# Performance work log

Measured on AMD Instinct MI355X. Metric: run time of the kernel, lower is better.

## Reference

```python
import jax, jax.numpy as jnp
import numpy as np
import math

B, S = 4, 1024
N_ITEMS, EMB = 50000, 128
H, D = 4, 32


def setup_inputs() -> dict:
    key = jax.random.key(0)
    ks = jax.random.split(key, 12)

    def lin(k, fan_in, fan_out):
        lim = 1.0 / math.sqrt(fan_in)
        return jax.random.uniform(k, (fan_in, fan_out), minval=-lim, maxval=lim, dtype=jnp.float32)

    inp = {}
    inp["sequence_item_indices"] = jax.random.randint(ks[0], (B, S), 0, N_ITEMS, dtype=jnp.int32)
    inp["sequence_correct_flags"] = jax.random.randint(ks[1], (B, S), 0, 2, dtype=jnp.int32)
    inp["sequence_time_gaps"] = jax.random.uniform(ks[2], (B, S), dtype=jnp.float32) * 100.0
    inp["item_emb"] = jax.random.normal(ks[3], (N_ITEMS, EMB), dtype=jnp.float32) * 0.02
    inp["ans_emb"] = jax.random.normal(ks[4], (2, EMB), dtype=jnp.float32) * 0.02
    inp["Wq"] = lin(ks[5], EMB, H * D); inp["bq"] = jnp.zeros((H * D,), jnp.float32)
    inp["Wk"] = lin(ks[6], EMB, H * D); inp["bk"] = jnp.zeros((H * D,), jnp.float32)
    inp["Wv"] = lin(ks[7], EMB, H * D); inp["bv"] = jnp.zeros((H * D,), jnp.float32)
    inp["Wh"] = lin(ks[8], 2 * EMB, EMB); inp["bh"] = jnp.zeros((EMB,), jnp.float32)
    inp["W1"] = lin(ks[9], H * D + EMB, EMB); inp["b1"] = jnp.zeros((EMB,), jnp.float32)
    inp["W2"] = lin(ks[10], EMB, 1); inp["b2"] = jnp.zeros((1,), jnp.float32)
    inp["theta_raw"] = jnp.zeros((H,), jnp.float32)
    return inp


def reference(sequence_item_indices, sequence_correct_flags, sequence_time_gaps,
              item_emb, ans_emb, Wq, bq, Wk, bk, Wv, bv, Wh, bh, W1, b1, W2, b2, theta_raw):
    Bb, Ss = sequence_item_indices.shape
    Hn = theta_raw.shape[0]
    Dd = Wq.shape[1] // Hn

    e = item_emb[sequence_item_indices]                      # [B,S,E]
    a = ans_emb[sequence_correct_flags]                      # [B,S,E]
    inter = jnp.concatenate([e, a], axis=-1) @ Wh + bh       # history_projection

    Q = (e @ Wq + bq).reshape(Bb, Ss, Hn, Dd)
    K = (e @ Wk + bk).reshape(Bb, Ss, Hn, Dd)
    V = (inter @ Wv + bv).reshape(Bb, Ss, Hn, Dd)
    scale = 1.0 / jnp.sqrt(jnp.float32(Dd))

    # self relevance per history position; per-target softmax over i<t done via exclusive prefix sums
    sr = jnp.sum(Q * K, axis=-1) * scale                     # [B,S,H]
    ex = jnp.exp(sr - jnp.max(sr, axis=1, keepdims=True))    # shift-invariant
    Ep = jnp.concatenate([jnp.zeros((Bb, 1, Hn), sr.dtype), jnp.cumsum(ex, axis=1)], axis=1)  # [B,S+1,H]

    g = jnp.maximum(sequence_time_gaps.astype(jnp.float32), 1.0)
    Pp = jnp.concatenate([jnp.zeros((Bb, 1), g.dtype), jnp.cumsum(g, axis=1)], axis=1)        # [B,S+1]

    t = jnp.arange(1, Ss)                                    # targets, T = S-1
    i = jnp.arange(Ss)                                       # history positions
    mask = i[None, :] < t[:, None]                           # [T,S]
    step = (t[:, None] - i[None, :]).astype(jnp.float32)     # arange(L,0,-1)[i] == t - i
    gap_diff = Pp[:, 1:Ss, None] - Pp[:, None, :Ss]          # [B,T,S]  sum_{j in [i,t)} clamp(gap,1)
    Et = Ep[:, 1:Ss, :]                                      # [B,T,H]  softmax normalizer Z_t
    rel = (Et[:, :, None, :] - Ep[:, None, :Ss, :]) / Et[:, :, None, :]  # cumulative relevance [B,T,S,H]
    pd = jnp.where(mask[None, :, :, None],
                   step[None, :, :, None] * gap_diff[..., None] * rel, 0.0)  # perceived distance

    theta = jax.nn.softplus(theta_raw) + 1e-4                # [H]
    decay = jnp.exp(-theta * pd)                             # [B,T,S,H]

    # candidate query at position t equals query_projection(item_embedding[t])
    raw = jnp.einsum('bthd,bihd->btih', Q[:, 1:], K) * scale # [B,T,S,H]
    scores = jnp.where(mask[None, :, :, None], raw * decay, -1e30)
    attn = jax.nn.softmax(scores, axis=2)                    # softmax over history positions
    ctx = jnp.einsum('btih,bihd->bthd', attn, V).reshape(Bb, Ss - 1, Hn * Dd)

    feat = jnp.concatenate([ctx, e[:, 1:]], axis=-1)
    h1 = jax.nn.relu(feat @ W1 + b1)                         # dropout is inference identity
    logit = (h1 @ W2 + b2)[..., 0]
    pred = jax.nn.sigmoid(logit)                             # [B,S-1]
    valid = jnp.ones((Bb, Ss - 1), dtype=bool)               # all positions valid (no padding)
    return pred, valid
```

## Files before the change

### kernel.cpp

```cpp
#include <hip/hip_runtime.h>
#include <math.h>

#define BSZ 4
#define SSZ 1024
#define EMBD 128
#define HN 4
#define DN 32
#define TQ (SSZ - 1)
#define NROWS (BSZ * TQ)

typedef __attribute__((ext_vector_type(8))) short bf16x8;
typedef __attribute__((ext_vector_type(4))) short bf16x4;
typedef __attribute__((ext_vector_type(4))) float f32x4;

static __device__ __forceinline__ unsigned short f2bf(float x) {
    union { float f; unsigned u; } v; v.f = x;
    unsigned r = v.u + 0x7fffu + ((v.u >> 16) & 1u);
    return (unsigned short)(r >> 16);
}
static __device__ __forceinline__ bf16x8 cvt8(const float4 a, const float4 b) {
    bf16x8 v;
    v[0] = (short)f2bf(a.x); v[1] = (short)f2bf(a.y);
    v[2] = (short)f2bf(a.z); v[3] = (short)f2bf(a.w);
    v[4] = (short)f2bf(b.x); v[5] = (short)f2bf(b.y);
    v[6] = (short)f2bf(b.z); v[7] = (short)f2bf(b.w);
    return v;
}

__global__ __launch_bounds__(256)
void embed4_kernel(const int* __restrict__ idx, const int* __restrict__ flg,
                   const float* __restrict__ item_emb, const float* __restrict__ ans_emb,
                   const float* __restrict__ Wq, const float* __restrict__ bq,
                   const float* __restrict__ Wk, const float* __restrict__ bk,
                   const float* __restrict__ Wv, const float* __restrict__ bv,
                   const float* __restrict__ Wh, const float* __restrict__ bh_bias,
                   unsigned short* __restrict__ Qts, unsigned short* __restrict__ Kts,
                   unsigned short* __restrict__ Vts,
                   float* __restrict__ ec, float* __restrict__ srw)
{
    __shared__ __align__(16) unsigned short esb[16][136];
    __shared__ __align__(16) unsigned short asb[16][136];
    __shared__ __align__(16) unsigned short intb[16][136];
    __shared__ __align__(16) unsigned short Wt[128][40];

    const int tid = threadIdx.x;
    const int tok0 = blockIdx.x * 16;
    const int b = blockIdx.x >> 6;
    const int s0 = tok0 & 1023;
    const int w = tid >> 6, lane = tid & 63;
    const int quad = lane >> 4, col = lane & 15;

    {
        const int tk = tid >> 4;
        const int d0 = (tid & 15) * 8;
        const int tok = tok0 + tk;
        const float* esrc = item_emb + (size_t)idx[tok] * EMBD + d0;
        const float* asrc = ans_emb + (size_t)flg[tok] * EMBD + d0;
        const float4 e0 = *(const float4*)esrc;
        const float4 e1 = *(const float4*)(esrc + 4);
        const float4 a0 = *(const float4*)asrc;
        const float4 a1 = *(const float4*)(asrc + 4);
        *(float4*)(ec + (size_t)tok * EMBD + d0) = e0;
        *(float4*)(ec + (size_t)tok * EMBD + d0 + 4) = e1;
        *(bf16x8*)&esb[tk][d0] = cvt8(e0, e1);
        *(bf16x8*)&asb[tk][d0] = cvt8(a0, a1);
    }

    const int jb = (tid & 31) * 4;
    const int ib = (tid >> 5) * 4;
    float rr[4][4];

    #define WSRC(R) ((R) < 8 ? Wh + (size_t)(R) * 4096                     \
                  : (R) < 12 ? Wq + (size_t)((R) - 8) * 4096               \
                  : (R) < 16 ? Wk + (size_t)((R) - 12) * 4096              \
                  : Wv + (size_t)((R) - 16) * 4096)
    #define LOADW(P)                                                       \
    {                                                                      \
        const float* _p = (P);                                             \
        *(float4*)rr[0] = *(const float4*)(_p + (ib + 0) * 128 + jb);      \
        *(float4*)rr[1] = *(const float4*)(_p + (ib + 1) * 128 + jb);      \
        *(float4*)rr[2] = *(const float4*)(_p + (ib + 2) * 128 + jb);      \
        *(float4*)rr[3] = *(const float4*)(_p + (ib + 3) * 128 + jb);      \
    }
    #define STOREW                                                         \
    {                                                                      \
        _Pragma("unroll")                                                  \
        for (int jj = 0; jj < 4; jj++) {                                   \
            bf16x4 v;                                                      \
            v[0] = (short)f2bf(rr[0][jj]); v[1] = (short)f2bf(rr[1][jj]);  \
            v[2] = (short)f2bf(rr[2][jj]); v[3] = (short)f2bf(rr[3][jj]);  \
            *(bf16x4*)&Wt[jb + jj][ib] = v;                                \
        }                                                                  \
    }

    f32x4 accI[2] = {{0.f,0.f,0.f,0.f},{0.f,0.f,0.f,0.f}};
    f32x4 accQ[2] = {{0.f,0.f,0.f,0.f},{0.f,0.f,0.f,0.f}};
    f32x4 accK[2] = {{0.f,0.f,0.f,0.f},{0.f,0.f,0.f,0.f}};
    f32x4 accV[2] = {{0.f,0.f,0.f,0.f},{0.f,0.f,0.f,0.f}};

    LOADW(WSRC(0));
    #pragma unroll
    for (int r = 0; r < 20; r++) {
        __syncthreads();
        STOREW;
        __syncthreads();
        if (r < 19) LOADW(WSRC(r + 1));

        const unsigned short (*Ab)[136] = (r < 4) ? esb : (r < 8) ? asb
                                        : (r < 16) ? esb : intb;
        const int koff = ((r < 8) ? (r & 3) : (r < 12) ? (r - 8)
                        : (r < 16) ? (r - 12) : (r - 16)) * 32;
        const bf16x8 af = *(const bf16x8*)&Ab[col][koff + quad * 8];
        f32x4* acc = (r < 8) ? accI : (r < 12) ? accQ : (r < 16) ? accK : accV;
        #pragma unroll
        for (int ntl = 0; ntl < 2; ntl++) {
            const bf16x8 bf = *(const bf16x8*)&Wt[w * 32 + ntl * 16 + col][quad * 8];
            acc[ntl] = __builtin_amdgcn_mfma_f32_16x16x32_bf16(af, bf, acc[ntl], 0, 0, 0);
        }
        if (r == 7) {
            #pragma unroll
            for (int ntl = 0; ntl < 2; ntl++) {
                const int j = w * 32 + ntl * 16 + col;
                const float bb = bh_bias[j];
                #pragma unroll
                for (int r4 = 0; r4 < 4; r4++)
                    intb[quad * 4 + r4][j] = f2bf(accI[ntl][r4] + bb);
            }
        }
    }
    #undef LOADW
    #undef STOREW
    #undef WSRC

    const int bhn = b * HN + w;
    const float scale = 0.17677669529663687f;
    float p[4] = {0.f, 0.f, 0.f, 0.f};
    #pragma unroll
    for (int ntl = 0; ntl < 2; ntl++) {
        const int j = w * 32 + ntl * 16 + col;
        const float bQ = bq[j], bK = bk[j], bV = bv[j];
        #pragma unroll
        for (int r = 0; r < 4; r++) {
            const float qv = accQ[ntl][r] + bQ;
            const float kv = accK[ntl][r] + bK;
            const int s = s0 + quad * 4 + r;
            const size_t o = ((size_t)bhn * SSZ + s) * DN + ntl * 16 + col;
            Qts[o] = f2bf(qv * scale);
            Kts[o] = f2bf(kv);
            Vts[o] = f2bf(accV[ntl][r] + bV);
            p[r] = fmaf(qv, kv, p[r]);
        }
    }
    #pragma unroll
    for (int r = 0; r < 4; r++) {
        float pr = p[r];
        pr += __shfl_xor(pr, 1, 64);
        pr += __shfl_xor(pr, 2, 64);
        pr += __shfl_xor(pr, 4, 64);
        pr += __shfl_xor(pr, 8, 64);
        if (col == 0)
            srw[(size_t)bhn * SSZ + s0 + quad * 4 + r] = pr * scale;
    }
}

__global__ __launch_bounds__(256)
void attn4_kernel(const unsigned short* __restrict__ Qts,
                  const unsigned short* __restrict__ Kts,
                  const unsigned short* __restrict__ Vts,
                  const float* __restrict__ srw, const float* __restrict__ gaps,
                  const float* __restrict__ theta_raw, float* __restrict__ csw)
{
    __shared__ __align__(16) unsigned short Ks[64][40];
    __shared__ __align__(16) unsigned short Vs[32][72];
    __shared__ __align__(16) unsigned short Ps[4][16][72];
    __shared__ float EpS[SSZ + 1];
    __shared__ float PpS[SSZ + 1];
    __shared__ float wtot[4];

    const int bid = blockIdx.x;
    const int qt = bid & 15;
    const int bh = bid >> 4;
    const int b = bh >> 2, h = bh & 3;
    const int tid = threadIdx.x;
    const int w = tid >> 6, lane = tid & 63;
    const int quad = lane >> 4, col = lane & 15;
    const int t0 = qt * 64 + 1;

    {
        const float4 sv = *(const float4*)(srw + (size_t)bh * SSZ + tid * 4);
        const float e0 = __expf(sv.x);
        const float p0 = e0;
        const float p1 = p0 + __expf(sv.y);
        const float p2 = p1 + __expf(sv.z);
        const float p3 = p2 + __expf(sv.w);
        float s = p3;
        #pragma unroll
        for (int d = 1; d < 64; d <<= 1) {
            const float t = __shfl_up(s, d, 64);
            if (lane >= d) s += t;
        }
        if (lane == 63) wtot[w] = s;
        __syncthreads();
        float base = s - p3;
        for (int ww = 0; ww < w; ww++) base += wtot[ww];
        EpS[tid * 4 + 1] = base + p0;
        EpS[tid * 4 + 2] = base + p1;
        EpS[tid * 4 + 3] = base + p2;
        EpS[tid * 4 + 4] = base + p3;
        if (tid == 0) EpS[0] = 0.0f;
    }
    {
        const float4 gv = *(const float4*)(gaps + (size_t)b * SSZ + tid * 4);
        const float p0 = fmaxf(gv.x, 1.0f);
        const float p1 = p0 + fmaxf(gv.y, 1.0f);
        const float p2 = p1 + fmaxf(gv.z, 1.0f);
        const float p3 = p2 + fmaxf(gv.w, 1.0f);
        float s = p3;
        #pragma unroll
        for (int d = 1; d < 64; d <<= 1) {
            const float t = __shfl_up(s, d, 64);
            if (lane >= d) s += t;
        }
        __syncthreads();
        if (lane == 63) wtot[w] = s;
        __syncthreads();
        float base = s - p3;
        for (int ww = 0; ww < w; ww++) base += wtot[ww];
        PpS[tid * 4 + 1] = base + p0;
        PpS[tid * 4 + 2] = base + p1;
        PpS[tid * 4 + 3] = base + p2;
        PpS[tid * 4 + 4] = base + p3;
        if (tid == 0) PpS[0] = 0.0f;
    }
    __syncthreads();

    const float theta = logf(1.0f + __expf(theta_raw[h])) + 1e-4f;
    const float nth = -theta;
    float Ept[4], Ppt[4], iEp[4], tft[4];
    int qrow[4], tq[4];
    #pragma unroll
    for (int r = 0; r < 4; r++) {
        qrow[r] = w * 16 + quad * 4 + r;
        tq[r] = t0 + qrow[r];
        tft[r] = (float)tq[r];
        Ept[r] = EpS[tq[r]];
        Ppt[r] = PpS[tq[r]];
        iEp[r] = 1.0f / Ept[r];
    }

    bf16x8 aq;
    {
        int t = t0 + w * 16 + col; if (t > 1023) t = 1023;
        aq = *(const bf16x8*)(Qts + ((size_t)(bh * SSZ + t)) * DN + quad * 8);
    }

    f32x4 acc0 = {0.f, 0.f, 0.f, 0.f};
    f32x4 acc1 = {0.f, 0.f, 0.f, 0.f};
    float lsum[4] = {0.f, 0.f, 0.f, 0.f};

    const int i_st = tid >> 2;
    const int d0 = (tid & 3) * 8;
    bf16x8 kreg = *(const bf16x8*)(Kts + ((size_t)(bh * SSZ + i_st)) * DN + d0);
    bf16x8 vreg = *(const bf16x8*)(Vts + ((size_t)(bh * SSZ + i_st)) * DN + d0);

    for (int c = 0; c <= qt; c++) {
        __syncthreads();
        *(bf16x8*)&Ks[i_st][d0] = kreg;
        #pragma unroll
        for (int k2 = 0; k2 < 8; k2++) Vs[d0 + k2][i_st] = (unsigned short)vreg[k2];
        __syncthreads();
        if (c < qt) {
            const size_t o = ((size_t)(bh * SSZ + (c + 1) * 64 + i_st)) * DN + d0;
            kreg = *(const bf16x8*)(Kts + o);
            vreg = *(const bf16x8*)(Vts + o);
        }

        const bool full = (c < qt);
        #pragma unroll
        for (int nt = 0; nt < 4; nt++) {
            const bf16x8 bk = *(const bf16x8*)&Ks[nt * 16 + col][quad * 8];
            f32x4 z = {0.f, 0.f, 0.f, 0.f};
            f32x4 raw = __builtin_amdgcn_mfma_f32_16x16x32_bf16(aq, bk, z, 0, 0, 0);
            const int il = nt * 16 + col;
            const int i_ = c * 64 + il;
            const float Epi = EpS[i_];
            const float Ppi = PpS[i_];
            const float fi = (float)i_;
            #pragma unroll
            for (int r = 0; r < 4; r++) {
                const float pdv = (tft[r] - fi) * (Ppt[r] - Ppi) * ((Ept[r] - Epi) * iEp[r]);
                const float sc  = raw[r] * __expf(nth * pdv);
                float p = __expf(sc);
                p = (full || il <= qrow[r]) ? p : 0.0f;
                lsum[r] += p;
                Ps[w][quad * 4 + r][il] = f2bf(p);
            }
        }
        #pragma unroll
        for (int ks = 0; ks < 2; ks++) {
            const bf16x8 ap = *(const bf16x8*)&Ps[w][col][ks * 32 + quad * 8];
            const bf16x8 bv0 = *(const bf16x8*)&Vs[col][ks * 32 + quad * 8];
            const bf16x8 bv1 = *(const bf16x8*)&Vs[16 + col][ks * 32 + quad * 8];
            acc0 = __builtin_amdgcn_mfma_f32_16x16x32_bf16(ap, bv0, acc0, 0, 0, 0);
            acc1 = __builtin_amdgcn_mfma_f32_16x16x32_bf16(ap, bv1, acc1, 0, 0, 0);
        }
    }

    #pragma unroll
    for (int r = 0; r < 4; r++) {
        float lr = lsum[r];
        #pragma unroll
        for (int msk = 8; msk >= 1; msk >>= 1) lr += __shfl_xor(lr, msk, 64);
        lsum[r] = 1.0f / lr;
    }
    #pragma unroll
    for (int r = 0; r < 4; r++) {
        if (tq[r] <= 1023) {
            float* dst = csw + ((size_t)(b * TQ + (tq[r] - 1))) * EMBD + h * DN;
            dst[col]      = acc0[r] * lsum[r];
            dst[16 + col] = acc1[r] * lsum[r];
        }
    }
}

__global__ __launch_bounds__(256)
void mlp3_kernel(const float* __restrict__ csw, const float* __restrict__ ec,
                 const float* __restrict__ W1, const float* __restrict__ b1,
                 const float* __restrict__ W2, const float* __restrict__ b2,
                 float* __restrict__ out)
{
    __shared__ __align__(16) unsigned short featb[32][264];
    __shared__ __align__(16) unsigned short W1t[128][264];
    __shared__ float sred[4][16];

    const int tid = threadIdx.x;
    const int r0 = blockIdx.x * 32;
    const int w = tid >> 6, lane = tid & 63;
    const int quad = lane >> 4, col = lane & 15;
    const int mt = w & 1, nh = w >> 1;

    {
        const int jb = (tid & 31) * 4;
        const int ib = (tid >> 5) * 4;
        for (int ic = 0; ic < 8; ic++) {
            const int i0 = ic * 32 + ib;
            float rr[4][4];
            *(float4*)rr[0] = *(const float4*)(W1 + (size_t)(i0 + 0) * 128 + jb);
            *(float4*)rr[1] = *(const float4*)(W1 + (size_t)(i0 + 1) * 128 + jb);
            *(float4*)rr[2] = *(const float4*)(W1 + (size_t)(i0 + 2) * 128 + jb);
            *(float4*)rr[3] = *(const float4*)(W1 + (size_t)(i0 + 3) * 128 + jb);
            #pragma unroll
            for (int jj = 0; jj < 4; jj++) {
                bf16x4 v;
                v[0] = (short)f2bf(rr[0][jj]); v[1] = (short)f2bf(rr[1][jj]);
                v[2] = (short)f2bf(rr[2][jj]); v[3] = (short)f2bf(rr[3][jj]);
                *(bf16x4*)&W1t[jb + jj][i0] = v;
            }
        }
    }
    {
        const int rr = tid >> 3;
        const int c0 = (tid & 7) * 32;
        int row = r0 + rr; if (row >= NROWS) row = NROWS - 1;
        const float* src;
        if (c0 < 128) {
            src = csw + (size_t)row * EMBD + c0;
        } else {
            const int bb = row / TQ;
            const int tt = row - bb * TQ + 1;
            src = ec + ((size_t)(bb * SSZ + tt)) * EMBD + (c0 - 128);
        }
        #pragma unroll
        for (int g = 0; g < 4; g++) {
            const float4 f0 = ((const float4*)src)[g * 2];
            const float4 f1 = ((const float4*)src)[g * 2 + 1];
            *(bf16x8*)&featb[rr][c0 + g * 8] = cvt8(f0, f1);
        }
    }
    __syncthreads();

    float s[4] = {0.f, 0.f, 0.f, 0.f};
    #pragma unroll
    for (int ntl = 0; ntl < 4; ntl++) {
        const int nt = nh * 4 + ntl;
        f32x4 acc = {0.f, 0.f, 0.f, 0.f};
        #pragma unroll
        for (int kc = 0; kc < 8; kc++) {
            const bf16x8 af = *(const bf16x8*)&featb[mt * 16 + col][kc * 32 + quad * 8];
            const bf16x8 bf = *(const bf16x8*)&W1t[nt * 16 + col][kc * 32 + quad * 8];
            acc = __builtin_amdgcn_mfma_f32_16x16x32_bf16(af, bf, acc, 0, 0, 0);
        }
        const int j = nt * 16 + col;
        const float b1j = b1[j], w2j = W2[j];
        #pragma unroll
        for (int r = 0; r < 4; r++)
            s[r] = fmaf(fmaxf(acc[r] + b1j, 0.0f), w2j, s[r]);
    }
    #pragma unroll
    for (int r = 0; r < 4; r++) {
        float sr = s[r];
        sr += __shfl_xor(sr, 1, 64);
        sr += __shfl_xor(sr, 2, 64);
        sr += __shfl_xor(sr, 4, 64);
        sr += __shfl_xor(sr, 8, 64);
        if (col == 0) sred[w][quad * 4 + r] = sr;
    }
    __syncthreads();
    if (tid < 32) {
        const int mt2 = tid >> 4, rr = tid & 15;
        const float logit = sred[mt2][rr] + sred[mt2 + 2][rr] + b2[0];
        const int grow = r0 + tid;
        if (grow < NROWS) {
            out[grow] = 1.0f / (1.0f + __expf(-logit));
            out[NROWS + grow] = 1.0f;
        }
    }
}

extern "C" void kernel_launch(void* const* d_in, const int* in_sizes, int n_in,
                              void* d_out, int out_size, void* d_ws, size_t ws_size,
                              hipStream_t stream)
{
    const int*   idx       = (const int*)d_in[0];
    const int*   flg       = (const int*)d_in[1];
    const float* gaps      = (const float*)d_in[2];
    const float* item_emb  = (const float*)d_in[3];
    const float* ans_emb   = (const float*)d_in[4];
    const float* Wq        = (const float*)d_in[5];
    const float* bq        = (const float*)d_in[6];
    const float* Wk        = (const float*)d_in[7];
    const float* bk        = (const float*)d_in[8];
    const float* Wv        = (const float*)d_in[9];
    const float* bv        = (const float*)d_in[10];
    const float* Wh        = (const float*)d_in[11];
    const float* bh        = (const float*)d_in[12];
    const float* W1        = (const float*)d_in[13];
    const float* b1        = (const float*)d_in[14];
    const float* W2        = (const float*)d_in[15];
    const float* b2        = (const float*)d_in[16];
    const float* theta_raw = (const float*)d_in[17];
    (void)in_sizes; (void)n_in; (void)ws_size;

    const size_t QKV = (size_t)BSZ * HN * SSZ * DN;
    unsigned short* Qts = (unsigned short*)d_ws;
    unsigned short* Kts = Qts + QKV;
    unsigned short* Vts = Kts + QKV;
    float* ec  = (float*)(Vts + QKV);
    float* srw = ec + (size_t)BSZ * SSZ * EMBD;
    float* csw = srw + (size_t)BSZ * HN * SSZ;

    float* out = (float*)d_out;

    embed4_kernel<<<BSZ * SSZ / 16, 256, 0, stream>>>(
        idx, flg, item_emb, ans_emb, Wq, bq, Wk, bk, Wv, bv, Wh, bh,
        Qts, Kts, Vts, ec, srw);
    attn4_kernel<<<BSZ * HN * 16, 256, 0, stream>>>(
        Qts, Kts, Vts, srw, gaps, theta_raw, csw);
    mlp3_kernel<<<(NROWS + 31) / 32, 256, 0, stream>>>(
        csw, ec, W1, b1, W2, b2, out);
}
```

Before: 149.4 us.

## Split attention key chunks across waves, double-buffer embed weights, shrink MLP tiles

The attention kernel no longer has all four waves share each 64-key chunk. Each wave now processes its own interleaved key chunks for all 64 queries of the block, with private K/V/P tiles, and the partial outputs and normalizers are merged through shared-memory atomics. This removes the per-chunk block-wide barriers and the serial chunk loop. The embed kernel double-buffers the transposed weight tile so there is one barrier per step instead of two, and the MLP kernel moves to 16-row tiles where each wave stages only its own slice of W1. The costs are more shared memory, LDS atomics, and W1 being converted twice as many times overall.

```diff
diff --git a/kernel.cpp b/kernel.cpp
--- a/kernel.cpp
+++ b/kernel.cpp
@@ -28,7 +28,7 @@
 }
 
 __global__ __launch_bounds__(256)
-void embed4_kernel(const int* __restrict__ idx, const int* __restrict__ flg,
+void embed5_kernel(const int* __restrict__ idx, const int* __restrict__ flg,
                    const float* __restrict__ item_emb, const float* __restrict__ ans_emb,
                    const float* __restrict__ Wq, const float* __restrict__ bq,
                    const float* __restrict__ Wk, const float* __restrict__ bk,
@@ -41,7 +41,7 @@
     __shared__ __align__(16) unsigned short esb[16][136];
     __shared__ __align__(16) unsigned short asb[16][136];
     __shared__ __align__(16) unsigned short intb[16][136];
-    __shared__ __align__(16) unsigned short Wt[128][40];
+    __shared__ __align__(16) unsigned short Wt[2][128][40];
 
     const int tid = threadIdx.x;
     const int tok0 = blockIdx.x * 16;
@@ -82,14 +82,14 @@
         *(float4*)rr[2] = *(const float4*)(_p + (ib + 2) * 128 + jb);      \
         *(float4*)rr[3] = *(const float4*)(_p + (ib + 3) * 128 + jb);      \
     }
-    #define STOREW                                                         \
+    #define STOREW(B)                                                      \
     {                                                                      \
         _Pragma("unroll")                                                  \
         for (int jj = 0; jj < 4; jj++) {                                   \
             bf16x4 v;                                                      \
             v[0] = (short)f2bf(rr[0][jj]); v[1] = (short)f2bf(rr[1][jj]);  \
             v[2] = (short)f2bf(rr[2][jj]); v[3] = (short)f2bf(rr[3][jj]);  \
-            *(bf16x4*)&Wt[jb + jj][ib] = v;                                \
+            *(bf16x4*)&Wt[B][jb + jj][ib] = v;                             \
         }                                                                  \
     }
 
@@ -99,11 +99,11 @@
     f32x4 accV[2] = {{0.f,0.f,0.f,0.f},{0.f,0.f,0.f,0.f}};
 
     LOADW(WSRC(0));
+    STOREW(0);
+    __syncthreads();
+
     #pragma unroll
     for (int r = 0; r < 20; r++) {
-        __syncthreads();
-        STOREW;
-        __syncthreads();
         if (r < 19) LOADW(WSRC(r + 1));
 
         const unsigned short (*Ab)[136] = (r < 4) ? esb : (r < 8) ? asb
@@ -114,7 +114,7 @@
         f32x4* acc = (r < 8) ? accI : (r < 12) ? accQ : (r < 16) ? accK : accV;
         #pragma unroll
         for (int ntl = 0; ntl < 2; ntl++) {
-            const bf16x8 bf = *(const bf16x8*)&Wt[w * 32 + ntl * 16 + col][quad * 8];
+            const bf16x8 bf = *(const bf16x8*)&Wt[r & 1][w * 32 + ntl * 16 + col][quad * 8];
             acc[ntl] = __builtin_amdgcn_mfma_f32_16x16x32_bf16(af, bf, acc[ntl], 0, 0, 0);
         }
         if (r == 7) {
@@ -127,6 +127,8 @@
                     intb[quad * 4 + r4][j] = f2bf(accI[ntl][r4] + bb);
             }
         }
+        if (r < 19) STOREW((r + 1) & 1);
+        __syncthreads();
     }
     #undef LOADW
     #undef STOREW
@@ -164,18 +166,19 @@
 }
 
 __global__ __launch_bounds__(256)
-void attn4_kernel(const unsigned short* __restrict__ Qts,
+void attn5_kernel(const unsigned short* __restrict__ Qts,
                   const unsigned short* __restrict__ Kts,
                   const unsigned short* __restrict__ Vts,
                   const float* __restrict__ srw, const float* __restrict__ gaps,
                   const float* __restrict__ theta_raw, float* __restrict__ csw)
 {
-    __shared__ __align__(16) unsigned short Ks[64][40];
-    __shared__ __align__(16) unsigned short Vs[32][72];
-    __shared__ __align__(16) unsigned short Ps[4][16][72];
+    __shared__ __align__(16) unsigned short Kw[4][64][40];
+    __shared__ __align__(16) unsigned short Vw[4][32][72];
+    __shared__ __align__(16) unsigned short Pw[4][64][72];
     __shared__ float EpS[SSZ + 1];
-    __shared__ float PpS[SSZ + 1];
+    __shared__ float PpS[SSZ + 2];
     __shared__ float wtot[4];
+    __shared__ float mrg[64][36];
 
     const int bid = blockIdx.x;
     const int qt = bid & 15;
@@ -186,10 +189,11 @@
     const int quad = lane >> 4, col = lane & 15;
     const int t0 = qt * 64 + 1;
 
+    for (int x = tid; x < 64 * 36; x += 256) ((float*)mrg)[x] = 0.0f;
+
     {
         const float4 sv = *(const float4*)(srw + (size_t)bh * SSZ + tid * 4);
-        const float e0 = __expf(sv.x);
-        const float p0 = e0;
+        const float p0 = __expf(sv.x);
         const float p1 = p0 + __expf(sv.y);
         const float p2 = p1 + __expf(sv.z);
         const float p3 = p2 + __expf(sv.w);
@@ -237,130 +241,144 @@
     const float theta = logf(1.0f + __expf(theta_raw[h])) + 1e-4f;
     const float nth = -theta;
     float Ept[4], Ppt[4], iEp[4], tft[4];
-    int qrow[4], tq[4];
-    #pragma unroll
-    for (int r = 0; r < 4; r++) {
-        qrow[r] = w * 16 + quad * 4 + r;
-        tq[r] = t0 + qrow[r];
-        tft[r] = (float)tq[r];
-        Ept[r] = EpS[tq[r]];
-        Ppt[r] = PpS[tq[r]];
-        iEp[r] = 1.0f / Ept[r];
-    }
-
-    bf16x8 aq;
-    {
-        int t = t0 + w * 16 + col; if (t > 1023) t = 1023;
-        aq = *(const bf16x8*)(Qts + ((size_t)(bh * SSZ + t)) * DN + quad * 8);
-    }
-
-    f32x4 acc0 = {0.f, 0.f, 0.f, 0.f};
-    f32x4 acc1 = {0.f, 0.f, 0.f, 0.f};
+    int qrow[4];
+    #pragma unroll
+    for (int nt = 0; nt < 4; nt++) {
+        qrow[nt] = nt * 16 + col;
+        const int t = t0 + qrow[nt];
+        tft[nt] = (float)t;
+        const int tc = (t <= 1023) ? t : 1023;
+        Ept[nt] = EpS[tc];
+        Ppt[nt] = PpS[tc];
+        iEp[nt] = 1.0f / Ept[nt];
+    }
+
+    bf16x8 bq[4];
+    #pragma unroll
+    for (int nt = 0; nt < 4; nt++) {
+        int t = t0 + nt * 16 + col; if (t > 1023) t = 1023;
+        bq[nt] = *(const bf16x8*)(Qts + ((size_t)(bh * SSZ + t)) * DN + quad * 8);
+    }
+
+    f32x4 acc[4][2];
+    #pragma unroll
+    for (int m = 0; m < 4; m++) { acc[m][0] = {0,0,0,0}; acc[m][1] = {0,0,0,0}; }
     float lsum[4] = {0.f, 0.f, 0.f, 0.f};
 
-    const int i_st = tid >> 2;
-    const int d0 = (tid & 3) * 8;
-    bf16x8 kreg = *(const bf16x8*)(Kts + ((size_t)(bh * SSZ + i_st)) * DN + d0);
-    bf16x8 vreg = *(const bf16x8*)(Vts + ((size_t)(bh * SSZ + i_st)) * DN + d0);
-
-    for (int c = 0; c <= qt; c++) {
-        __syncthreads();
-        *(bf16x8*)&Ks[i_st][d0] = kreg;
-        #pragma unroll
-        for (int k2 = 0; k2 < 8; k2++) Vs[d0 + k2][i_st] = (unsigned short)vreg[k2];
-        __syncthreads();
-        if (c < qt) {
-            const size_t o = ((size_t)(bh * SSZ + (c + 1) * 64 + i_st)) * DN + d0;
-            kreg = *(const bf16x8*)(Kts + o);
-            vreg = *(const bf16x8*)(Vts + o);
+    bf16x8 kpre[4], vpre[4];
+    {
+        const size_t o = ((size_t)(bh * SSZ + w * 64 + lane)) * DN;
+        #pragma unroll
+        for (int j = 0; j < 4; j++) {
+            kpre[j] = *(const bf16x8*)(Kts + o + j * 8);
+            vpre[j] = *(const bf16x8*)(Vts + o + j * 8);
+        }
+    }
+
+    for (int c = w; c <= qt; c += 4) {
+        #pragma unroll
+        for (int j = 0; j < 4; j++) *(bf16x8*)&Kw[w][lane][j * 8] = kpre[j];
+        #pragma unroll
+        for (int j = 0; j < 4; j++)
+            #pragma unroll
+            for (int k = 0; k < 8; k++) Vw[w][j * 8 + k][lane] = (unsigned short)vpre[j][k];
+        if (c + 4 <= qt) {
+            const size_t o = ((size_t)(bh * SSZ + (c + 4) * 64 + lane)) * DN;
+            #pragma unroll
+            for (int j = 0; j < 4; j++) {
+                kpre[j] = *(const bf16x8*)(Kts + o + j * 8);
+                vpre[j] = *(const bf16x8*)(Vts + o + j * 8);
+            }
         }
 
         const bool full = (c < qt);
         #pragma unroll
-        for (int nt = 0; nt < 4; nt++) {
-            const bf16x8 bk = *(const bf16x8*)&Ks[nt * 16 + col][quad * 8];
-            f32x4 z = {0.f, 0.f, 0.f, 0.f};
-            f32x4 raw = __builtin_amdgcn_mfma_f32_16x16x32_bf16(aq, bk, z, 0, 0, 0);
-            const int il = nt * 16 + col;
-            const int i_ = c * 64 + il;
-            const float Epi = EpS[i_];
-            const float Ppi = PpS[i_];
-            const float fi = (float)i_;
+        for (int mt = 0; mt < 4; mt++) {
+            const bf16x8 af = *(const bf16x8*)&Kw[w][mt * 16 + col][quad * 8];
+            f32x4 raw[4];
+            #pragma unroll
+            for (int nt = 0; nt < 4; nt++) {
+                f32x4 z = {0.f, 0.f, 0.f, 0.f};
+                raw[nt] = __builtin_amdgcn_mfma_f32_16x16x32_bf16(af, bq[nt], z, 0, 0, 0);
+            }
             #pragma unroll
             for (int r = 0; r < 4; r++) {
-                const float pdv = (tft[r] - fi) * (Ppt[r] - Ppi) * ((Ept[r] - Epi) * iEp[r]);
-                const float sc  = raw[r] * __expf(nth * pdv);
-                float p = __expf(sc);
-                p = (full || il <= qrow[r]) ? p : 0.0f;
-                lsum[r] += p;
-                Ps[w][quad * 4 + r][il] = f2bf(p);
-            }
-        }
-        #pragma unroll
-        for (int ks = 0; ks < 2; ks++) {
-            const bf16x8 ap = *(const bf16x8*)&Ps[w][col][ks * 32 + quad * 8];
-            const bf16x8 bv0 = *(const bf16x8*)&Vs[col][ks * 32 + quad * 8];
-            const bf16x8 bv1 = *(const bf16x8*)&Vs[16 + col][ks * 32 + quad * 8];
-            acc0 = __builtin_amdgcn_mfma_f32_16x16x32_bf16(ap, bv0, acc0, 0, 0, 0);
-            acc1 = __builtin_amdgcn_mfma_f32_16x16x32_bf16(ap, bv1, acc1, 0, 0, 0);
-        }
-    }
-
-    #pragma unroll
-    for (int r = 0; r < 4; r++) {
-        float lr = lsum[r];
-        #pragma unroll
-        for (int msk = 8; msk >= 1; msk >>= 1) lr += __shfl_xor(lr, msk, 64);
-        lsum[r] = 1.0f / lr;
-    }
-    #pragma unroll
-    for (int r = 0; r < 4; r++) {
-        if (tq[r] <= 1023) {
-            float* dst = csw + ((size_t)(b * TQ + (tq[r] - 1))) * EMBD + h * DN;
-            dst[col]      = acc0[r] * lsum[r];
-            dst[16 + col] = acc1[r] * lsum[r];
+                const int kl = mt * 16 + quad * 4 + r;
+                const int i_ = c * 64 + kl;
+                const float Epi = EpS[i_];
+                const float Ppi = PpS[i_];
+                const float fi = (float)i_;
+                #pragma unroll
+                for (int nt = 0; nt < 4; nt++) {
+                    const float pdv = (tft[nt] - fi) * (Ppt[nt] - Ppi)
+                                    * ((Ept[nt] - Epi) * iEp[nt]);
+                    const float sc = raw[nt][r] * __expf(nth * pdv);
+                    float p = __expf(sc);
+                    p = (full || kl <= qrow[nt]) ? p : 0.0f;
+                    lsum[nt] += p;
+                    Pw[w][nt * 16 + col][kl] = f2bf(p);
+                }
+            }
+        }
+        #pragma unroll
+        for (int mtq = 0; mtq < 4; mtq++) {
+            #pragma unroll
+            for (int kc = 0; kc < 2; kc++) {
+                const bf16x8 ap = *(const bf16x8*)&Pw[w][mtq * 16 + col][kc * 32 + quad * 8];
+                const bf16x8 bv0 = *(const bf16x8*)&Vw[w][col][kc * 32 + quad * 8];
+                const bf16x8 bv1 = *(const bf16x8*)&Vw[w][16 + col][kc * 32 + quad * 8];
+                acc[mtq][0] = __builtin_amdgcn_mfma_f32_16x16x32_bf16(ap, bv0, acc[mtq][0], 0, 0, 0);
+                acc[mtq][1] = __builtin_amdgcn_mfma_f32_16x16x32_bf16(ap, bv1, acc[mtq][1], 0, 0, 0);
+            }
+        }
+    }
+
+    #pragma unroll
+    for (int nt = 0; nt < 4; nt++) {
+        float l = lsum[nt];
+        l += __shfl_xor(l, 16, 64);
+        l += __shfl_xor(l, 32, 64);
+        if (quad == 0) atomicAdd(&mrg[nt * 16 + col][32], l);
+    }
+    #pragma unroll
+    for (int mtq = 0; mtq < 4; mtq++)
+        #pragma unroll
+        for (int ntv = 0; ntv < 2; ntv++)
+            #pragma unroll
+            for (int r = 0; r < 4; r++)
+                atomicAdd(&mrg[mtq * 16 + quad * 4 + r][ntv * 16 + col], acc[mtq][ntv][r]);
+    __syncthreads();
+
+    {
+        const int q = tid >> 2, dg = tid & 3;
+        const int t = t0 + q;
+        if (t <= 1023) {
+            const float inv = 1.0f / mrg[q][32];
+            float* dst = csw + ((size_t)(b * TQ + (t - 1))) * EMBD + h * DN + dg * 8;
+            #pragma unroll
+            for (int d = 0; d < 8; d++) dst[d] = mrg[q][dg * 8 + d] * inv;
         }
     }
 }
 
 __global__ __launch_bounds__(256)
-void mlp3_kernel(const float* __restrict__ csw, const float* __restrict__ ec,
+void mlp4_kernel(const float* __restrict__ csw, const float* __restrict__ ec,
                  const float* __restrict__ W1, const float* __restrict__ b1,
                  const float* __restrict__ W2, const float* __restrict__ b2,
                  float* __restrict__ out)
 {
-    __shared__ __align__(16) unsigned short featb[32][264];
-    __shared__ __align__(16) unsigned short W1t[128][264];
+    __shared__ __align__(16) unsigned short featb[16][264];
+    __shared__ __align__(16) unsigned short W1q[4][32][264];
     __shared__ float sred[4][16];
 
     const int tid = threadIdx.x;
-    const int r0 = blockIdx.x * 32;
+    const int r0 = blockIdx.x * 16;
     const int w = tid >> 6, lane = tid & 63;
     const int quad = lane >> 4, col = lane & 15;
-    const int mt = w & 1, nh = w >> 1;
-
-    {
-        const int jb = (tid & 31) * 4;
-        const int ib = (tid >> 5) * 4;
-        for (int ic = 0; ic < 8; ic++) {
-            const int i0 = ic * 32 + ib;
-            float rr[4][4];
-            *(float4*)rr[0] = *(const float4*)(W1 + (size_t)(i0 + 0) * 128 + jb);
-            *(float4*)rr[1] = *(const float4*)(W1 + (size_t)(i0 + 1) * 128 + jb);
-            *(float4*)rr[2] = *(const float4*)(W1 + (size_t)(i0 + 2) * 128 + jb);
-            *(float4*)rr[3] = *(const float4*)(W1 + (size_t)(i0 + 3) * 128 + jb);
-            #pragma unroll
-            for (int jj = 0; jj < 4; jj++) {
-                bf16x4 v;
-                v[0] = (short)f2bf(rr[0][jj]); v[1] = (short)f2bf(rr[1][jj]);
-                v[2] = (short)f2bf(rr[2][jj]); v[3] = (short)f2bf(rr[3][jj]);
-                *(bf16x4*)&W1t[jb + jj][i0] = v;
-            }
-        }
-    }
-    {
-        const int rr = tid >> 3;
-        const int c0 = (tid & 7) * 32;
+
+    {
+        const int rr = tid >> 4;
+        const int c0 = (tid & 15) * 16;
         int row = r0 + rr; if (row >= NROWS) row = NROWS - 1;
         const float* src;
         if (c0 < 128) {
@@ -370,27 +388,47 @@
             const int tt = row - bb * TQ + 1;
             src = ec + ((size_t)(bb * SSZ + tt)) * EMBD + (c0 - 128);
         }
-        #pragma unroll
-        for (int g = 0; g < 4; g++) {
-            const float4 f0 = ((const float4*)src)[g * 2];
-            const float4 f1 = ((const float4*)src)[g * 2 + 1];
-            *(bf16x8*)&featb[rr][c0 + g * 8] = cvt8(f0, f1);
+        const float4 f0 = ((const float4*)src)[0];
+        const float4 f1 = ((const float4*)src)[1];
+        const float4 f2 = ((const float4*)src)[2];
+        const float4 f3 = ((const float4*)src)[3];
+        *(bf16x8*)&featb[rr][c0]     = cvt8(f0, f1);
+        *(bf16x8*)&featb[rr][c0 + 8] = cvt8(f2, f3);
+    }
+
+    {
+        const int jl = (lane & 7) * 4;
+        const int ib2 = (lane >> 3) * 4;
+        const int jg = w * 32 + jl;
+        for (int ic = 0; ic < 8; ic++) {
+            const int i0 = ic * 32 + ib2;
+            float rr[4][4];
+            *(float4*)rr[0] = *(const float4*)(W1 + (size_t)(i0 + 0) * 128 + jg);
+            *(float4*)rr[1] = *(const float4*)(W1 + (size_t)(i0 + 1) * 128 + jg);
+            *(float4*)rr[2] = *(const float4*)(W1 + (size_t)(i0 + 2) * 128 + jg);
+            *(float4*)rr[3] = *(const float4*)(W1 + (size_t)(i0 + 3) * 128 + jg);
+            #pragma unroll
+            for (int jj = 0; jj < 4; jj++) {
+                bf16x4 v;
+                v[0] = (short)f2bf(rr[0][jj]); v[1] = (short)f2bf(rr[1][jj]);
+                v[2] = (short)f2bf(rr[2][jj]); v[3] = (short)f2bf(rr[3][jj]);
+                *(bf16x4*)&W1q[w][jl + jj][i0] = v;
+            }
         }
     }
     __syncthreads();
 
     float s[4] = {0.f, 0.f, 0.f, 0.f};
     #pragma unroll
-    for (int ntl = 0; ntl < 4; ntl++) {
-        const int nt = nh * 4 + ntl;
+    for (int ntl = 0; ntl < 2; ntl++) {
         f32x4 acc = {0.f, 0.f, 0.f, 0.f};
         #pragma unroll
         for (int kc = 0; kc < 8; kc++) {
-            const bf16x8 af = *(const bf16x8*)&featb[mt * 16 + col][kc * 32 + quad * 8];
-            const bf16x8 bf = *(const bf16x8*)&W1t[nt * 16 + col][kc * 32 + quad * 8];
+            const bf16x8 af = *(const bf16x8*)&featb[col][kc * 32 + quad * 8];
+            const bf16x8 bf = *(const bf16x8*)&W1q[w][ntl * 16 + col][kc * 32 + quad * 8];
             acc = __builtin_amdgcn_mfma_f32_16x16x32_bf16(af, bf, acc, 0, 0, 0);
         }
-        const int j = nt * 16 + col;
+        const int j = w * 32 + ntl * 16 + col;
         const float b1j = b1[j], w2j = W2[j];
         #pragma unroll
         for (int r = 0; r < 4; r++)
@@ -406,9 +444,9 @@
         if (col == 0) sred[w][quad * 4 + r] = sr;
     }
     __syncthreads();
-    if (tid < 32) {
-        const int mt2 = tid >> 4, rr = tid & 15;
-        const float logit = sred[mt2][rr] + sred[mt2 + 2][rr] + b2[0];
+    if (tid < 16) {
+        const float logit = sred[0][tid] + sred[1][tid] + sred[2][tid]
+                          + sred[3][tid] + b2[0];
         const int grow = r0 + tid;
         if (grow < NROWS) {
             out[grow] = 1.0f / (1.0f + __expf(-logit));
@@ -451,11 +489,11 @@
 
     float* out = (float*)d_out;
 
-    embed4_kernel<<<BSZ * SSZ / 16, 256, 0, stream>>>(
+    embed5_kernel<<<BSZ * SSZ / 16, 256, 0, stream>>>(
         idx, flg, item_emb, ans_emb, Wq, bq, Wk, bk, Wv, bv, Wh, bh,
         Qts, Kts, Vts, ec, srw);
-    attn4_kernel<<<BSZ * HN * 16, 256, 0, stream>>>(
+    attn5_kernel<<<BSZ * HN * 16, 256, 0, stream>>>(
         Qts, Kts, Vts, srw, gaps, theta_raw, csw);
-    mlp3_kernel<<<(NROWS + 31) / 32, 256, 0, stream>>>(
+    mlp4_kernel<<<(NROWS + 15) / 16, 256, 0, stream>>>(
         csw, ec, W1, b1, W2, b2, out);
 }
```

New measurement: 151.6 us. About the same (+1.4%).
